# Kernel optimization log

Hardware: AMD Instinct MI355X
Metric: run time of the kernel (lower is better)

The kernel has to match this reference:

```python
import jax, jax.numpy as jnp
import numpy as np


def _conv(x, w, b):
    # torch Conv2d stride=2, padding=1, kernel=3; w: [out,in,3,3]
    y = jax.lax.conv_general_dilated(x, w, (2, 2), ((1, 1), (1, 1)),
                                     dimension_numbers=('NCHW', 'OIHW', 'NCHW'))
    return y + b[None, :, None, None]


def _deconv(x, w, b):
    # torch ConvTranspose2d stride=2, padding=1, output_padding=1, kernel=3
    # torch weight layout: [in, out, kH, kW] -> flip spatial, swap to OIHW
    wt = jnp.flip(w, (2, 3)).transpose(1, 0, 2, 3)
    y = jax.lax.conv_general_dilated(x, wt, (1, 1), ((1, 2), (1, 2)),
                                     lhs_dilation=(2, 2),
                                     dimension_numbers=('NCHW', 'OIHW', 'NCHW'))
    return y + b[None, :, None, None]


def _forward(x, conv1_w, conv1_b, conv2_w, conv2_b, conv3_w, conv3_b, conv4_w, conv4_b,
             l2_w, l2_b, cl_w, cl_b, n_w, n_b, low, high,
             l4_w, l4_b, lL_w, lL_b, fc4_w, fc4_b, fc5_w, fc5_b,
             dc1_w, dc1_b, dc2_w, dc2_b, dc3_w, dc3_b, dc4_w, dc4_b):
    relu = jax.nn.relu
    lrelu = lambda t: jax.nn.leaky_relu(t, 0.01)
    h = relu(_conv(x, conv1_w, conv1_b))    # [B,16,64,64]
    h = relu(_conv(h, conv2_w, conv2_b))    # [B,8,32,32]
    h = relu(_conv(h, conv3_w, conv3_b))    # [B,4,16,16]
    h = relu(_conv(h, conv4_w, conv4_b))    # [B,2,8,8]
    B = h.shape[0]
    h = h.reshape(B, -1)                    # [B,128]
    h = relu(h @ l2_w.T + l2_b)             # [B,256]
    # CustomLayer: Linear(256,512) + 512 batched RangeTanhNeurons
    lin = h @ cl_w.T + cl_b                              # [B,512]
    neur = jnp.tanh(jnp.tanh(low * (h @ n_w.T + n_b) - high))  # [B,512]
    h = relu(lin + neur)
    h = relu(h @ l4_w.T + l4_b)             # [B,256]
    h = lrelu(h @ lL_w.T + lL_b)            # [B,256]
    h = lrelu(h @ fc4_w.T + fc4_b)          # [B,512]
    h = relu(h @ fc5_w.T + fc5_b)           # [B,512]
    h = h.reshape(B, 8, 8, 8)
    h = _deconv(h, dc1_w, dc1_b)            # [B,16,16,16]
    h = _deconv(h, dc2_w, dc2_b)            # [B,32,32,32]
    h = _deconv(h, dc3_w, dc3_b)            # [B,64,64,64]
    h = _deconv(h, dc4_w, dc4_b)            # [B,3,128,128]
    return h


def setup_inputs() -> dict:
    key = jax.random.key(0)
    ks = iter(jax.random.split(key, 64))
    f32 = jnp.float32

    def n(shape, s=0.05):
        return jax.random.normal(next(ks), shape, f32) * s

    def z(c):
        return jnp.zeros((c,), f32)

    inp = {
        'x': jax.random.normal(next(ks), (256, 3, 128, 128), f32),
        'conv1_w': n((16, 3, 3, 3)), 'conv1_b': z(16),
        'conv2_w': n((8, 16, 3, 3)), 'conv2_b': z(8),
        'conv3_w': n((4, 8, 3, 3)), 'conv3_b': z(4),
        'conv4_w': n((2, 4, 3, 3)), 'conv4_b': z(2),
        'l2_w': n((256, 128)), 'l2_b': z(256),
        'cl_w': n((512, 256)), 'cl_b': z(512),
        'n_w': n((512, 256)), 'n_b': z(512),
        'low': jax.random.uniform(next(ks), (512,), f32) * 10000.0,
        'high': jax.random.uniform(next(ks), (512,), f32) * 10.0,
        'l4_w': n((256, 512)), 'l4_b': z(256),
        'lL_w': n((256, 256)), 'lL_b': z(256),
        'fc4_w': n((512, 256)), 'fc4_b': z(512),
        'fc5_w': n((512, 512)), 'fc5_b': z(512),
        'dc1_w': n((8, 16, 3, 3)), 'dc1_b': z(16),
        'dc2_w': n((16, 32, 3, 3)), 'dc2_b': z(32),
        'dc3_w': n((32, 64, 3, 3)), 'dc3_b': z(64),
        'dc4_w': n((64, 3, 3, 3)), 'dc4_b': z(3),
    }
    return inp


def reference(x, conv1_w, conv1_b, conv2_w, conv2_b, conv3_w, conv3_b, conv4_w, conv4_b,
              l2_w, l2_b, cl_w, cl_b, n_w, n_b, low, high,
              l4_w, l4_b, lL_w, lL_b, fc4_w, fc4_b, fc5_w, fc5_b,
              dc1_w, dc1_b, dc2_w, dc2_b, dc3_w, dc3_b, dc4_w, dc4_b):
    return _forward(x, conv1_w, conv1_b, conv2_w, conv2_b, conv3_w, conv3_b, conv4_w, conv4_b,
                    l2_w, l2_b, cl_w, cl_b, n_w, n_b, low, high,
                    l4_w, l4_b, lL_w, lL_b, fc4_w, fc4_b, fc5_w, fc5_b,
                    dc1_w, dc1_b, dc2_w, dc2_b, dc3_w, dc3_b, dc4_w, dc4_b)
```

## Files before the change

kernel.cpp:

```cpp
#include <hip/hip_runtime.h>
#include <hip/hip_bf16.h>
#include <math.h>


template <int IC, int OC, int IH, int IW>
__global__ __launch_bounds__(256) void conv_k(const float* __restrict__ x,
                                              const float* __restrict__ w,
                                              const float* __restrict__ b,
                                              float* __restrict__ y, int B) {
    constexpr int OH = IH / 2, OW = IW / 2;
    __shared__ float wlds[IC * 9 * OC];
    for (int t = threadIdx.x; t < IC * 9 * OC; t += blockDim.x) {
        int oc = t % OC;
        int r = t / OC;
        int tap = r % 9;
        int ic = r / 9;
        wlds[t] = w[(oc * IC + ic) * 9 + tap];
    }
    __syncthreads();

    int idx = blockIdx.x * blockDim.x + threadIdx.x;
    if (idx >= B * OH * OW) return;
    int ox = idx % OW;
    int t2 = idx / OW;
    int oy = t2 % OH;
    int n = t2 / OH;

    const float* xn = x + (size_t)n * IC * IH * IW;
    float acc[OC];
#pragma unroll
    for (int oc = 0; oc < OC; oc++) acc[oc] = b[oc];

#pragma unroll 2
    for (int ic = 0; ic < IC; ic++) {
        float xv[9];
#pragma unroll
        for (int ky = 0; ky < 3; ky++) {
            int iy = 2 * oy - 1 + ky;
#pragma unroll
            for (int kx = 0; kx < 3; kx++) {
                int ix = 2 * ox - 1 + kx;
                bool ok = (iy >= 0) && (iy < IH) && (ix >= 0) && (ix < IW);
                xv[ky * 3 + kx] = ok ? xn[((size_t)ic * IH + iy) * IW + ix] : 0.f;
            }
        }
#pragma unroll
        for (int t3 = 0; t3 < 9; t3++) {
            if constexpr (OC % 4 == 0) {
                const float4* wr = (const float4*)(wlds + ((size_t)ic * 9 + t3) * OC);
#pragma unroll
                for (int o4 = 0; o4 < OC / 4; o4++) {
                    float4 wv = wr[o4];
                    acc[4 * o4 + 0] = fmaf(xv[t3], wv.x, acc[4 * o4 + 0]);
                    acc[4 * o4 + 1] = fmaf(xv[t3], wv.y, acc[4 * o4 + 1]);
                    acc[4 * o4 + 2] = fmaf(xv[t3], wv.z, acc[4 * o4 + 2]);
                    acc[4 * o4 + 3] = fmaf(xv[t3], wv.w, acc[4 * o4 + 3]);
                }
            } else {
#pragma unroll
                for (int oc = 0; oc < OC; oc++)
                    acc[oc] = fmaf(xv[t3], wlds[(ic * 9 + t3) * OC + oc], acc[oc]);
            }
        }
    }
    float* yn = y + (size_t)n * OC * OH * OW + (size_t)oy * OW + ox;
#pragma unroll
    for (int oc = 0; oc < OC; oc++) yn[(size_t)oc * OH * OW] = fmaxf(acc[oc], 0.f);
}

template <int IC, int OC, int OCH, int IH>
__global__ __launch_bounds__(256, 2) void deconv_full_k(const float* __restrict__ x,
                                                        const float* __restrict__ w,
                                                        const float* __restrict__ bias,
                                                        float* __restrict__ y, int B) {
    constexpr int IW = IH, OH = 2 * IH, OW = 2 * IH;
    __shared__ float wlds[IC * 9 * OCH];
    const int ocb = blockIdx.y * OCH;
    for (int t = threadIdx.x; t < IC * 9 * OCH; t += blockDim.x) {
        int oc = t % OCH;
        int r = t / OCH;
        int tap = r % 9;
        int ic = r / 9;
        wlds[t] = w[((size_t)(ic * OC + ocb + oc)) * 9 + tap];
    }
    __syncthreads();

    int idx = blockIdx.x * blockDim.x + threadIdx.x;
    if (idx >= B * IH * IW) return;
    int j = idx % IW;
    int t2 = idx / IW;
    int i = t2 % IH;
    int n = t2 / IH;

    const float* xn = x + (size_t)n * IC * IH * IW;
    float acc[2][2][OCH];
#pragma unroll
    for (int oc = 0; oc < OCH; oc++) {
        float bv = bias[ocb + oc];
        acc[0][0][oc] = bv;
        acc[0][1][oc] = bv;
        acc[1][0][oc] = bv;
        acc[1][1][oc] = bv;
    }
    const bool jok = (j + 1 < IW);

    constexpr int EDY[9] = {0, 0, 0, 0, 0, 0, 1, 1, 1};
    constexpr int EDX[9] = {0, 0, 0, 0, 1, 1, 0, 0, 1};
    constexpr int ERY[9] = {0, 0, 1, 1, 0, 1, 1, 1, 1};
    constexpr int ERX[9] = {0, 1, 0, 1, 1, 1, 0, 1, 1};
    constexpr int ETAP[9] = {4, 5, 7, 8, 3, 6, 1, 2, 0};

#pragma unroll 2
    for (int ic = 0; ic < IC; ic++) {
        const float* r0p = xn + ((size_t)ic * IH + i) * IW + j;
        const bool iok = (i + 1 < IH);
        float xv[2][2];
        xv[0][0] = r0p[0];
        xv[0][1] = jok ? r0p[1] : 0.f;
        xv[1][0] = iok ? r0p[IW] : 0.f;
        xv[1][1] = (iok && jok) ? r0p[IW + 1] : 0.f;
#pragma unroll
        for (int e = 0; e < 9; e++) {
            float xval = xv[EDY[e]][EDX[e]];
            const float4* wr = (const float4*)(wlds + ((size_t)ic * 9 + ETAP[e]) * OCH);
#pragma unroll
            for (int o4 = 0; o4 < OCH / 4; o4++) {
                float4 wv = wr[o4];
                acc[ERY[e]][ERX[e]][4 * o4 + 0] = fmaf(xval, wv.x, acc[ERY[e]][ERX[e]][4 * o4 + 0]);
                acc[ERY[e]][ERX[e]][4 * o4 + 1] = fmaf(xval, wv.y, acc[ERY[e]][ERX[e]][4 * o4 + 1]);
                acc[ERY[e]][ERX[e]][4 * o4 + 2] = fmaf(xval, wv.z, acc[ERY[e]][ERX[e]][4 * o4 + 2]);
                acc[ERY[e]][ERX[e]][4 * o4 + 3] = fmaf(xval, wv.w, acc[ERY[e]][ERX[e]][4 * o4 + 3]);
            }
        }
    }
    float* yb = y + ((size_t)(n * OC + ocb) * OH + 2 * i) * OW + 2 * j;
#pragma unroll
    for (int oc = 0; oc < OCH; oc++) {
        float* yp = yb + (size_t)oc * OH * OW;
        *reinterpret_cast<float2*>(yp) = make_float2(acc[0][0][oc], acc[0][1][oc]);
        *reinterpret_cast<float2*>(yp + OW) = make_float2(acc[1][0][oc], acc[1][1][oc]);
    }
}

__global__ __launch_bounds__(256) void repack3_k(const float* __restrict__ w,
                                                 float* __restrict__ dst) {
    int idx = blockIdx.x * blockDim.x + threadIdx.x;
    if (idx >= 32 * 64 * 9) return;
    int t = idx % 9;
    int r = idx / 9;
    dst[r * 12 + t] = w[idx];
}

__global__ __launch_bounds__(256, 2) void deconv3_k(const float* __restrict__ x,
                                                    const float* __restrict__ wrp,
                                                    const float* __restrict__ bias,
                                                    float* __restrict__ y,
                                                    int B) {
    constexpr int IC = 32, IH = 32, IW = 32, OC = 64, OH = 64, OW = 64;
    const int lane = threadIdx.x & 63;
    const int wv = __builtin_amdgcn_readfirstlane(threadIdx.x >> 6);
    const int row = blockIdx.x * 4 + wv;
    const int n = row >> 5;
    const int i = row & 31;
    if (n >= B) return;

    float acc[2][OW];
    const float bv = bias[lane];
#pragma unroll
    for (int c = 0; c < OW; c++) {
        acc[0][c] = bv;
        acc[1][c] = bv;
    }

    const float* xb = x + ((size_t)n * IC * IH + i) * IW;
    const bool rok = (i + 1 < IH);

    for (int ic = 0; ic < IC; ic++) {
        const float* xr = xb + (size_t)ic * IH * IW;
        float x0[IW];
#pragma unroll
        for (int j = 0; j < IW; j++) x0[j] = xr[j];

        const float* wl = wrp + ((size_t)ic * OC + lane) * 12;
        float w[9];
#pragma unroll
        for (int t = 0; t < 9; t++) w[t] = wl[t];

#pragma unroll
        for (int j = 0; j < IW; j++) {
            acc[0][2 * j] = fmaf(x0[j], w[4], acc[0][2 * j]);
            acc[0][2 * j + 1] = fmaf(x0[j], w[5], acc[0][2 * j + 1]);
            acc[1][2 * j] = fmaf(x0[j], w[7], acc[1][2 * j]);
            acc[1][2 * j + 1] = fmaf(x0[j], w[8], acc[1][2 * j + 1]);
            if (j >= 1) {
                acc[0][2 * j - 1] = fmaf(x0[j], w[3], acc[0][2 * j - 1]);
                acc[1][2 * j - 1] = fmaf(x0[j], w[6], acc[1][2 * j - 1]);
            }
        }
        if (rok) {
            float x1[IW];
#pragma unroll
            for (int j = 0; j < IW; j++) x1[j] = xr[IW + j];
#pragma unroll
            for (int j = 0; j < IW; j++) {
                acc[1][2 * j] = fmaf(x1[j], w[1], acc[1][2 * j]);
                acc[1][2 * j + 1] = fmaf(x1[j], w[2], acc[1][2 * j + 1]);
                if (j >= 1) acc[1][2 * j - 1] = fmaf(x1[j], w[0], acc[1][2 * j - 1]);
            }
        }
    }

    float* yb = y + ((size_t)(n * OC + lane) * OH + 2 * i) * OW;
#pragma unroll
    for (int r = 0; r < 2; r++)
#pragma unroll
        for (int c4 = 0; c4 < OW / 4; c4++)
            *reinterpret_cast<float4*>(yb + r * OW + 4 * c4) =
                make_float4(acc[r][4 * c4], acc[r][4 * c4 + 1], acc[r][4 * c4 + 2],
                            acc[r][4 * c4 + 3]);
}

__global__ __launch_bounds__(256, 4) void deconv_last_k(const float* __restrict__ x,
                                                        const float* __restrict__ w,
                                                        const float* __restrict__ bias,
                                                        float* __restrict__ y, int B) {
    constexpr int IC = 64, OCR = 3, IH = 64, IW = 64, OH = 128, OW = 128, JP = 32;
    __shared__ float wlds[IC * 9 * 4];
    for (int t = threadIdx.x; t < IC * 9 * 4; t += blockDim.x) {
        int oc = t % 4;
        int rest = t / 4;
        int tap = rest % 9;
        int ic = rest / 9;
        wlds[t] = (oc < OCR) ? w[(ic * OCR + oc) * 9 + tap] : 0.f;
    }
    __syncthreads();

    int idx = blockIdx.x * blockDim.x + threadIdx.x;
    if (idx >= B * IH * JP) return;
    int jp = idx % JP;
    int t2 = idx / JP;
    int i = t2 % IH;
    int n = t2 / IH;

    const float* xn = x + (size_t)n * IC * IH * IW + 2 * jp;
    float b0 = bias[0], b1 = bias[1], b2 = bias[2];
    float acc[2][4][4];
#pragma unroll
    for (int ry = 0; ry < 2; ry++)
#pragma unroll
        for (int c = 0; c < 4; c++) {
            acc[ry][c][0] = b0;
            acc[ry][c][1] = b1;
            acc[ry][c][2] = b2;
            acc[ry][c][3] = 0.f;
        }
    const bool jok = (jp + 1 < JP);

    constexpr int RDY[3] = {0, 0, 1};
    constexpr int RRY[3] = {0, 1, 1};
    constexpr int RKY[3] = {1, 2, 0};

#pragma unroll 4
    for (int ic = 0; ic < IC; ic++) {
        float xr[2][3];
#pragma unroll
        for (int r = 0; r < 2; r++) {
            const float* rp = xn + ((size_t)ic * IH + i + r) * IW;
            bool rok = (r == 0) || (i + 1 < IH);
            xr[r][0] = rok ? rp[0] : 0.f;
            xr[r][1] = rok ? rp[1] : 0.f;
            xr[r][2] = (rok && jok) ? rp[2] : 0.f;
        }
        const float4* w4 = (const float4*)(wlds) + ic * 9;
#pragma unroll
        for (int rc = 0; rc < 3; rc++) {
            float4 W0 = w4[RKY[rc] * 3 + 0];
            float4 W1 = w4[RKY[rc] * 3 + 1];
            float4 W2 = w4[RKY[rc] * 3 + 2];
            float x0 = xr[RDY[rc]][0], x1 = xr[RDY[rc]][1], x2 = xr[RDY[rc]][2];
#define QQ(c, xa, Wv)                                            \
    {                                                            \
        acc[RRY[rc]][c][0] = fmaf(xa, Wv.x, acc[RRY[rc]][c][0]); \
        acc[RRY[rc]][c][1] = fmaf(xa, Wv.y, acc[RRY[rc]][c][1]); \
        acc[RRY[rc]][c][2] = fmaf(xa, Wv.z, acc[RRY[rc]][c][2]); \
        acc[RRY[rc]][c][3] = fmaf(xa, Wv.w, acc[RRY[rc]][c][3]); \
    }
            QQ(0, x0, W1)
            QQ(1, x0, W2)
            QQ(1, x1, W0)
            QQ(2, x1, W1)
            QQ(3, x1, W2)
            QQ(3, x2, W0)
#undef QQ
        }
    }
#pragma unroll
    for (int oc = 0; oc < OCR; oc++) {
        float* yp = y + ((size_t)(n * OCR + oc) * OH + 2 * i) * OW + 4 * jp;
        *reinterpret_cast<float4*>(yp) =
            make_float4(acc[0][0][oc], acc[0][1][oc], acc[0][2][oc], acc[0][3][oc]);
        *reinterpret_cast<float4*>(yp + OW) =
            make_float4(acc[1][0][oc], acc[1][1][oc], acc[1][2][oc], acc[1][3][oc]);
    }
}

template <int IN, int OUT, int ACT>
__global__ __launch_bounds__(256) void linear_k(const float* __restrict__ h,
                                                const float* __restrict__ w,
                                                const float* __restrict__ b,
                                                float* __restrict__ y, int B) {
    int idx = blockIdx.x * blockDim.x + threadIdx.x;
    if (idx >= B * OUT) return;
    int o = idx % OUT;
    int n = idx / OUT;
    const float4* hr = (const float4*)(h + (size_t)n * IN);
    const float4* wr = (const float4*)(w + (size_t)o * IN);
    float acc = 0.f;
#pragma unroll 4
    for (int k = 0; k < IN / 4; k++) {
        float4 a = hr[k];
        float4 ww = wr[k];
        acc += a.x * ww.x + a.y * ww.y + a.z * ww.z + a.w * ww.w;
    }
    acc += b[o];
    y[idx] = (ACT == 0) ? fmaxf(acc, 0.f) : (acc > 0.f ? acc : 0.01f * acc);
}

__global__ __launch_bounds__(256) void custom_layer_k(
    const float* __restrict__ h, const float* __restrict__ clw, const float* __restrict__ clb,
    const float* __restrict__ nw, const float* __restrict__ nb, const float* __restrict__ low,
    const float* __restrict__ high, float* __restrict__ y, int B) {
    int idx = blockIdx.x * blockDim.x + threadIdx.x;
    if (idx >= B * 512) return;
    int o = idx % 512;
    int n = idx / 512;
    const float4* hr = (const float4*)(h + (size_t)n * 256);
    const float4* w1 = (const float4*)(clw + (size_t)o * 256);
    const float4* w2 = (const float4*)(nw + (size_t)o * 256);
    float lin = 0.f, z = 0.f;
#pragma unroll 4
    for (int k = 0; k < 64; k++) {
        float4 a = hr[k];
        float4 b1 = w1[k];
        float4 b2 = w2[k];
        lin += a.x * b1.x + a.y * b1.y + a.z * b1.z + a.w * b1.w;
        z += a.x * b2.x + a.y * b2.y + a.z * b2.z + a.w * b2.w;
    }
    lin += clb[o];
    z += nb[o];
    float neur = tanhf(tanhf(low[o] * z - high[o]));
    y[idx] = fmaxf(lin + neur, 0.f);
}

extern "C" void kernel_launch(void* const* d_in, const int* in_sizes, int n_in,
                              void* d_out, int out_size, void* d_ws, size_t ws_size,
                              hipStream_t stream) {
    const float* x = (const float*)d_in[0];
    const float* conv1_w = (const float*)d_in[1];
    const float* conv1_b = (const float*)d_in[2];
    const float* conv2_w = (const float*)d_in[3];
    const float* conv2_b = (const float*)d_in[4];
    const float* conv3_w = (const float*)d_in[5];
    const float* conv3_b = (const float*)d_in[6];
    const float* conv4_w = (const float*)d_in[7];
    const float* conv4_b = (const float*)d_in[8];
    const float* l2_w = (const float*)d_in[9];
    const float* l2_b = (const float*)d_in[10];
    const float* cl_w = (const float*)d_in[11];
    const float* cl_b = (const float*)d_in[12];
    const float* n_w = (const float*)d_in[13];
    const float* n_b = (const float*)d_in[14];
    const float* low = (const float*)d_in[15];
    const float* high = (const float*)d_in[16];
    const float* l4_w = (const float*)d_in[17];
    const float* l4_b = (const float*)d_in[18];
    const float* lL_w = (const float*)d_in[19];
    const float* lL_b = (const float*)d_in[20];
    const float* fc4_w = (const float*)d_in[21];
    const float* fc4_b = (const float*)d_in[22];
    const float* fc5_w = (const float*)d_in[23];
    const float* fc5_b = (const float*)d_in[24];
    const float* dc1_w = (const float*)d_in[25];
    const float* dc1_b = (const float*)d_in[26];
    const float* dc2_w = (const float*)d_in[27];
    const float* dc2_b = (const float*)d_in[28];
    const float* dc3_w = (const float*)d_in[29];
    const float* dc3_b = (const float*)d_in[30];
    const float* dc4_w = (const float*)d_in[31];
    const float* dc4_b = (const float*)d_in[32];

    const int B = in_sizes[0] / (3 * 128 * 128);
    float* out = (float*)d_out;
    float* ws = (float*)d_ws;

    float* rp3 = ws;
    float* h4 = rp3 + 24576;
    float* h5 = h4 + (size_t)B * 128;
    float* h6 = h5 + (size_t)B * 256;
    float* h7 = h6 + (size_t)B * 512;
    float* h8 = h7 + (size_t)B * 256;
    float* h9 = h8 + (size_t)B * 256;
    float* h10 = h9 + (size_t)B * 512;
    float* Rb = h10 + (size_t)B * 512;
    float* h1 = Rb;
    float* h2 = h1 + (size_t)B * 65536;
    float* h3 = h2 + (size_t)B * 8192;
    float* d1 = Rb;
    float* d3buf = Rb + (size_t)B * 4096;
    float* d2 = out + (size_t)B * (49152 - 32768);

    dim3 blk(256);
    auto cdiv = [](int a, int b) { return (a + b - 1) / b; };

    repack3_k<<<dim3(cdiv(32 * 64 * 9, 256)), blk, 0, stream>>>(dc3_w, rp3);

    conv_k<3, 16, 128, 128><<<dim3(cdiv(B * 64 * 64, 256)), blk, 0, stream>>>(x, conv1_w, conv1_b,
                                                                              h1, B);
    conv_k<16, 8, 64, 64><<<dim3(cdiv(B * 32 * 32, 256)), blk, 0, stream>>>(h1, conv2_w, conv2_b,
                                                                            h2, B);
    conv_k<8, 4, 32, 32><<<dim3(cdiv(B * 16 * 16, 256)), blk, 0, stream>>>(h2, conv3_w, conv3_b,
                                                                           h3, B);
    conv_k<4, 2, 16, 16><<<dim3(cdiv(B * 8 * 8, 256)), blk, 0, stream>>>(h3, conv4_w, conv4_b, h4,
                                                                         B);

    linear_k<128, 256, 0><<<dim3(cdiv(B * 256, 256)), blk, 0, stream>>>(h4, l2_w, l2_b, h5, B);
    custom_layer_k<<<dim3(cdiv(B * 512, 256)), blk, 0, stream>>>(h5, cl_w, cl_b, n_w, n_b, low,
                                                                 high, h6, B);
    linear_k<512, 256, 0><<<dim3(cdiv(B * 256, 256)), blk, 0, stream>>>(h6, l4_w, l4_b, h7, B);
    linear_k<256, 256, 1><<<dim3(cdiv(B * 256, 256)), blk, 0, stream>>>(h7, lL_w, lL_b, h8, B);
    linear_k<256, 512, 1><<<dim3(cdiv(B * 512, 256)), blk, 0, stream>>>(h8, fc4_w, fc4_b, h9, B);
    linear_k<512, 512, 0><<<dim3(cdiv(B * 512, 256)), blk, 0, stream>>>(h9, fc5_w, fc5_b, h10, B);

    deconv_full_k<8, 16, 8, 8><<<dim3(cdiv(B * 64, 256), 2), blk, 0, stream>>>(h10, dc1_w, dc1_b,
                                                                               d1, B);
    deconv_full_k<16, 32, 16, 16><<<dim3(cdiv(B * 256, 256), 2), blk, 0, stream>>>(d1, dc2_w,
                                                                                   dc2_b, d2, B);
    const int HB = B / 2;
    for (int c = 0; c < 2; c++) {
        const float* d2c = d2 + (size_t)c * HB * 32768;
        deconv3_k<<<dim3(HB * 32 / 4), blk, 0, stream>>>(d2c, rp3, dc3_b, d3buf, HB);
        deconv_last_k<<<dim3(cdiv(HB * 64 * 32, 256)), blk, 0, stream>>>(
            d3buf, dc4_w, dc4_b, out + (size_t)c * HB * 49152, HB);
    }
}
```

Measured before the change: 864.7 us.

## Split deconv3 rows into column halves per wave and chunk batch into quarters

Each wave of deconv3_k now computes half of an output row pair (32 columns) instead of the full 64. This halves the accumulator registers, which allows launch bounds of 4 waves per SIMD instead of 2. The two x-row loops are merged with zero-padding at the boundaries, and a halo column is loaded for the split. Batch chunking for the deconv3/deconv_last pair goes from 2 to 4 chunks, which shrinks the intermediate buffer footprint but adds launches.

```diff
diff --git a/kernel.cpp b/kernel.cpp
--- a/kernel.cpp
+++ b/kernel.cpp
@@ -151,7 +151,7 @@
     dst[r * 12 + t] = w[idx];
 }
 
-__global__ __launch_bounds__(256, 2) void deconv3_k(const float* __restrict__ x,
+__global__ __launch_bounds__(256, 4) void deconv3_k(const float* __restrict__ x,
                                                     const float* __restrict__ wrp,
                                                     const float* __restrict__ bias,
                                                     float* __restrict__ y,
@@ -159,62 +159,61 @@
     constexpr int IC = 32, IH = 32, IW = 32, OC = 64, OH = 64, OW = 64;
     const int lane = threadIdx.x & 63;
     const int wv = __builtin_amdgcn_readfirstlane(threadIdx.x >> 6);
-    const int row = blockIdx.x * 4 + wv;
+    const int wid = blockIdx.x * 4 + wv;
+    const int h = wid & 1;
+    const int row = wid >> 1;
     const int n = row >> 5;
     const int i = row & 31;
     if (n >= B) return;
 
-    float acc[2][OW];
+    float acc[2][32];
     const float bv = bias[lane];
 #pragma unroll
-    for (int c = 0; c < OW; c++) {
+    for (int c = 0; c < 32; c++) {
         acc[0][c] = bv;
         acc[1][c] = bv;
     }
 
-    const float* xb = x + ((size_t)n * IC * IH + i) * IW;
+    const float* xb = x + ((size_t)n * IC * IH + i) * IW + 16 * h;
     const bool rok = (i + 1 < IH);
 
     for (int ic = 0; ic < IC; ic++) {
         const float* xr = xb + (size_t)ic * IH * IW;
-        float x0[IW];
-#pragma unroll
-        for (int j = 0; j < IW; j++) x0[j] = xr[j];
-
+        float x0[17], x1[17];
+#pragma unroll
+        for (int jl = 0; jl <= 16; jl++) {
+            bool ok = (16 * h + jl < IW);
+            x0[jl] = ok ? xr[jl] : 0.f;
+            x1[jl] = (ok && rok) ? xr[IW + jl] : 0.f;
+        }
         const float* wl = wrp + ((size_t)ic * OC + lane) * 12;
-        float w[9];
-#pragma unroll
-        for (int t = 0; t < 9; t++) w[t] = wl[t];
-
-#pragma unroll
-        for (int j = 0; j < IW; j++) {
-            acc[0][2 * j] = fmaf(x0[j], w[4], acc[0][2 * j]);
-            acc[0][2 * j + 1] = fmaf(x0[j], w[5], acc[0][2 * j + 1]);
-            acc[1][2 * j] = fmaf(x0[j], w[7], acc[1][2 * j]);
-            acc[1][2 * j + 1] = fmaf(x0[j], w[8], acc[1][2 * j + 1]);
-            if (j >= 1) {
-                acc[0][2 * j - 1] = fmaf(x0[j], w[3], acc[0][2 * j - 1]);
-                acc[1][2 * j - 1] = fmaf(x0[j], w[6], acc[1][2 * j - 1]);
+        float w0 = wl[0], w1 = wl[1], w2 = wl[2], w3 = wl[3], w4 = wl[4], w5 = wl[5], w6 = wl[6],
+              w7 = wl[7], w8 = wl[8];
+#pragma unroll
+        for (int jl = 0; jl < 16; jl++) {
+            float xa = x0[jl], xc = x1[jl];
+            acc[0][2 * jl] = fmaf(xa, w4, acc[0][2 * jl]);
+            acc[0][2 * jl + 1] = fmaf(xa, w5, acc[0][2 * jl + 1]);
+            acc[1][2 * jl] = fmaf(xa, w7, acc[1][2 * jl]);
+            acc[1][2 * jl + 1] = fmaf(xa, w8, acc[1][2 * jl + 1]);
+            acc[1][2 * jl] = fmaf(xc, w1, acc[1][2 * jl]);
+            acc[1][2 * jl + 1] = fmaf(xc, w2, acc[1][2 * jl + 1]);
+            if (jl >= 1) {
+                acc[0][2 * jl - 1] = fmaf(xa, w3, acc[0][2 * jl - 1]);
+                acc[1][2 * jl - 1] = fmaf(xa, w6, acc[1][2 * jl - 1]);
+                acc[1][2 * jl - 1] = fmaf(xc, w0, acc[1][2 * jl - 1]);
             }
         }
-        if (rok) {
-            float x1[IW];
-#pragma unroll
-            for (int j = 0; j < IW; j++) x1[j] = xr[IW + j];
-#pragma unroll
-            for (int j = 0; j < IW; j++) {
-                acc[1][2 * j] = fmaf(x1[j], w[1], acc[1][2 * j]);
-                acc[1][2 * j + 1] = fmaf(x1[j], w[2], acc[1][2 * j + 1]);
-                if (j >= 1) acc[1][2 * j - 1] = fmaf(x1[j], w[0], acc[1][2 * j - 1]);
-            }
-        }
-    }
-
-    float* yb = y + ((size_t)(n * OC + lane) * OH + 2 * i) * OW;
+        acc[0][31] = fmaf(x0[16], w3, acc[0][31]);
+        acc[1][31] = fmaf(x0[16], w6, acc[1][31]);
+        acc[1][31] = fmaf(x1[16], w0, acc[1][31]);
+    }
+
+    float* yb = y + ((size_t)(n * OC + lane) * OH + 2 * i) * OW + 32 * h;
 #pragma unroll
     for (int r = 0; r < 2; r++)
 #pragma unroll
-        for (int c4 = 0; c4 < OW / 4; c4++)
+        for (int c4 = 0; c4 < 8; c4++)
             *reinterpret_cast<float4*>(yb + r * OW + 4 * c4) =
                 make_float4(acc[r][4 * c4], acc[r][4 * c4 + 1], acc[r][4 * c4 + 2],
                             acc[r][4 * c4 + 3]);
@@ -435,10 +434,11 @@
                                                                                d1, B);
     deconv_full_k<16, 32, 16, 16><<<dim3(cdiv(B * 256, 256), 2), blk, 0, stream>>>(d1, dc2_w,
                                                                                    dc2_b, d2, B);
-    const int HB = B / 2;
-    for (int c = 0; c < 2; c++) {
+    const int NCH = 4;
+    const int HB = B / NCH;
+    for (int c = 0; c < NCH; c++) {
         const float* d2c = d2 + (size_t)c * HB * 32768;
-        deconv3_k<<<dim3(HB * 32 / 4), blk, 0, stream>>>(d2c, rp3, dc3_b, d3buf, HB);
+        deconv3_k<<<dim3(HB * 32 * 2 / 4), blk, 0, stream>>>(d2c, rp3, dc3_b, d3buf, HB);
         deconv_last_k<<<dim3(cdiv(HB * 64 * 32, 256)), blk, 0, stream>>>(
             d3buf, dc4_w, dc4_b, out + (size_t)c * HB * 49152, HB);
     }
```

Result: no change. 877.0 us (+1.4%).
